# Kernel optimization log

Measured on AMD Instinct MI355X. Metric: run time of the kernel, lower is better.

Reference implementation:

```python
import jax, jax.numpy as jnp
import numpy as np

N, E, B, D, F_IN, E_IN, H = 8192, 32768, 256, 64, 11, 5, 128


def setup_inputs() -> dict:
    key = jax.random.key(0)
    ks = jax.random.split(key, 32)
    rn = lambda k, shape, s: jax.random.normal(k, shape, jnp.float32) * s
    inp = {
        'x': jax.random.normal(ks[0], (N, F_IN), jnp.float32),
        'edge_attr': jax.random.uniform(ks[1], (E, E_IN), jnp.float32),
        'lin0_w': rn(ks[2], (D, F_IN), 0.3), 'lin0_b': jnp.zeros((D,), jnp.float32),
        'nn1_w': rn(ks[3], (H, E_IN), 0.4), 'nn1_b': jnp.zeros((H,), jnp.float32),
        'nn2_w': rn(ks[4], (D * D, H), 0.05), 'nn2_b': jnp.zeros((D * D,), jnp.float32),
        'root_w': rn(ks[5], (D, D), 0.125), 'conv_b': jnp.zeros((D,), jnp.float32),
        'gru_w_ih': rn(ks[6], (3 * D, D), 0.125), 'gru_w_hh': rn(ks[7], (3 * D, D), 0.125),
        'gru_b_ih': jnp.zeros((3 * D,), jnp.float32), 'gru_b_hh': jnp.zeros((3 * D,), jnp.float32),
        's2s_w_ih': rn(ks[8], (4 * D, 2 * D), 0.1), 's2s_w_hh': rn(ks[9], (4 * D, D), 0.125),
        's2s_b_ih': jnp.zeros((4 * D,), jnp.float32), 's2s_b_hh': jnp.zeros((4 * D,), jnp.float32),
        'lin1_w': rn(ks[10], (D, 2 * D), 0.1), 'lin1_b': jnp.zeros((D,), jnp.float32),
        'lin2_w': rn(ks[11], (1, D), 0.125), 'lin2_b': jnp.zeros((1,), jnp.float32),
        'edge_index': jax.random.randint(ks[12], (2, E), 0, N),
        'batch': jnp.sort(jax.random.randint(ks[13], (N,), 0, B)),
    }
    return inp


def _forward(x, edge_attr, lin0_w, lin0_b, nn1_w, nn1_b, nn2_w, nn2_b, root_w, conv_b,
             gru_w_ih, gru_w_hh, gru_b_ih, gru_b_hh, s2s_w_ih, s2s_w_hh, s2s_b_ih, s2s_b_hh,
             lin1_w, lin1_b, lin2_w, lin2_b, edge_index, batch):
    src, dst = edge_index[0], edge_index[1]
    # edge-conditioned weights: MLP(edge_attr) -> [E, D, D]; edge_attr is fixed,
    # so compute once (identical math to calling conv.nn each iteration)
    W_e = (jax.nn.relu(edge_attr @ nn1_w.T + nn1_b) @ nn2_w.T + nn2_b).reshape(E, D, D)
    deg = jax.ops.segment_sum(jnp.ones((E,), jnp.float32), dst, num_segments=N)
    inv_deg = jnp.where(deg > 0, 1.0 / jnp.maximum(deg, 1.0), 0.0)[:, None]  # [N,1]

    out = jax.nn.relu(x @ lin0_w.T + lin0_b)  # [N, D]
    h = out
    for _ in range(3):
        # NNConv: gather src features, per-edge matmul, scatter-mean to dst, + root + bias
        msg = jnp.einsum('ed,edf->ef', out[src], W_e)  # [E, D]
        agg = jax.ops.segment_sum(msg, dst, num_segments=N) * inv_deg
        m = jax.nn.relu(agg + out @ root_w.T + conv_b)
        # single-step GRU (torch GRU equations)
        gx = m @ gru_w_ih.T + gru_b_ih
        gh = h @ gru_w_hh.T + gru_b_hh
        xr, xz, xn = jnp.split(gx, 3, axis=-1)
        hr, hz, hn = jnp.split(gh, 3, axis=-1)
        r = jax.nn.sigmoid(xr + hr)
        z = jax.nn.sigmoid(xz + hz)
        n = jnp.tanh(xn + r * hn)
        h = (1.0 - z) * n + z * h
        out = h

    # Set2Set pooling, 3 processing steps
    qh = jnp.zeros((B, D), jnp.float32)
    qc = jnp.zeros((B, D), jnp.float32)
    q_star = jnp.zeros((B, 2 * D), jnp.float32)
    for _ in range(3):
        gates = q_star @ s2s_w_ih.T + s2s_b_ih + qh @ s2s_w_hh.T + s2s_b_hh
        gi, gf, gg, go = jnp.split(gates, 4, axis=-1)
        qc = jax.nn.sigmoid(gf) * qc + jax.nn.sigmoid(gi) * jnp.tanh(gg)
        qh = jax.nn.sigmoid(go) * jnp.tanh(qc)
        q = qh  # [B, D]
        e = jnp.sum(out * q[batch], axis=-1)  # [N]
        emax = jax.ops.segment_max(e, batch, num_segments=B)
        emax = jnp.where(jnp.isfinite(emax), emax, 0.0)
        a = jnp.exp(e - emax[batch])
        a_sum = jax.ops.segment_sum(a, batch, num_segments=B)
        a = a / jnp.maximum(a_sum, 1e-12)[batch]
        r_vec = jax.ops.segment_sum(a[:, None] * out, batch, num_segments=B)  # [B, D]
        q_star = jnp.concatenate([q, r_vec], axis=-1)

    y = jax.nn.relu(q_star @ lin1_w.T + lin1_b) @ lin2_w.T + lin2_b
    return y.reshape(-1)  # [B]


def reference(x, edge_attr, lin0_w, lin0_b, nn1_w, nn1_b, nn2_w, nn2_b, root_w, conv_b,
              gru_w_ih, gru_w_hh, gru_b_ih, gru_b_hh, s2s_w_ih, s2s_w_hh, s2s_b_ih, s2s_b_hh,
              lin1_w, lin1_b, lin2_w, lin2_b, edge_index, batch):
    return _forward(x, edge_attr, lin0_w, lin0_b, nn1_w, nn1_b, nn2_w, nn2_b, root_w, conv_b,
                    gru_w_ih, gru_w_hh, gru_b_ih, gru_b_hh, s2s_w_ih, s2s_w_hh, s2s_b_ih, s2s_b_hh,
                    lin1_w, lin1_b, lin2_w, lin2_b, edge_index, batch)
```

## Files before the change

kernel.cpp:

```cpp
#include <hip/hip_runtime.h>
#include <hip/hip_bf16.h>
#include <stdint.h>

#define NN 8192
#define EE 32768
#define BB 256
#define DD 64
#define FIN 11
#define EIN 5
#define HH 128

typedef __attribute__((ext_vector_type(4))) float f32x4;
typedef __attribute__((ext_vector_type(8))) short bf16x8;

__device__ __forceinline__ float sigmoidf_(float x) { return 1.0f / (1.0f + expf(-x)); }

__device__ __forceinline__ void gload16(const void* g, void* l) {
    __builtin_amdgcn_global_load_lds(
        (const __attribute__((address_space(1))) unsigned int*)g,
        (__attribute__((address_space(3))) unsigned int*)l, 16, 0, 0);
}

__global__ __launch_bounds__(256) void k_setup(const float* __restrict__ x,
                                               const float* __restrict__ edge_attr,
                                               const float* __restrict__ lin0_w,
                                               const float* __restrict__ lin0_b,
                                               const float* __restrict__ nn1_w,
                                               const float* __restrict__ nn1_b,
                                               const float* __restrict__ nn2_w,
                                               const float* __restrict__ nn2b,
                                               const float* __restrict__ root_w,
                                               const float* __restrict__ whh,
                                               const float* __restrict__ bhh,
                                               const float* __restrict__ s2s_wih,
                                               const float* __restrict__ s2s_whh,
                                               const int* __restrict__ ei,
                                               const int* __restrict__ batch,
                                               __hip_bfloat16* __restrict__ h1,
                                               float* __restrict__ outN,
                                               __hip_bfloat16* __restrict__ nn2T,
                                               float* __restrict__ wihT,
                                               float* __restrict__ whhT,
                                               float* __restrict__ Bcat,
                                               float* __restrict__ bcat,
                                               int* __restrict__ deg,
                                               int* __restrict__ cnt) {
    const int bid = blockIdx.x, t = threadIdx.x;
    if (bid < 4096) {
        int u = bid * 256 + t;
        int e = u >> 5, k0 = (u & 31) * 4;
        float ea0 = edge_attr[e * EIN + 0], ea1 = edge_attr[e * EIN + 1],
              ea2 = edge_attr[e * EIN + 2], ea3 = edge_attr[e * EIN + 3],
              ea4 = edge_attr[e * EIN + 4];
        ushort4 o;
#pragma unroll
        for (int kk = 0; kk < 4; kk++) {
            int k = k0 + kk;
            const float* wr = nn1_w + k * EIN;
            float a = nn1_b[k] + ea0 * wr[0] + ea1 * wr[1] + ea2 * wr[2] + ea3 * wr[3] + ea4 * wr[4];
            __hip_bfloat16 b = __float2bfloat16(fmaxf(a, 0.0f));
            ((ushort*)&o)[kk] = *(ushort*)&b;
        }
        *(ushort4*)((ushort*)h1 + (size_t)e * 128 + k0) = o;
    } else if (bid < 4608) {
        int u = (bid - 4096) * 256 + t;
        int n = u >> 4, d0 = (u & 15) * 4;
        float xv[FIN];
#pragma unroll
        for (int k = 0; k < FIN; k++) xv[k] = x[n * FIN + k];
        float4 o;
#pragma unroll
        for (int dd = 0; dd < 4; dd++) {
            int d = d0 + dd;
            const float* wr = lin0_w + d * FIN;
            float a = lin0_b[d];
#pragma unroll
            for (int k = 0; k < FIN; k++) a += xv[k] * wr[k];
            ((float*)&o)[dd] = fmaxf(a, 0.0f);
        }
        *(float4*)(outN + (size_t)n * 64 + d0) = o;
    } else if (bid < 4864) {
        int u = (bid - 4608) * 256 + t;
        int d = u >> 10, rem = u & 1023, slot = rem >> 6, f = rem & 63;
        const float* src = nn2_w + ((size_t)(d * 64 + f) * 128 + slot * 8);
        float4 v0 = *(const float4*)(src);
        float4 v1 = *(const float4*)(src + 4);
        union { bf16x8 v; ushort us[8]; } ov;
        __hip_bfloat16 b;
        b = __float2bfloat16(v0.x); ov.us[0] = *(ushort*)&b;
        b = __float2bfloat16(v0.y); ov.us[1] = *(ushort*)&b;
        b = __float2bfloat16(v0.z); ov.us[2] = *(ushort*)&b;
        b = __float2bfloat16(v0.w); ov.us[3] = *(ushort*)&b;
        b = __float2bfloat16(v1.x); ov.us[4] = *(ushort*)&b;
        b = __float2bfloat16(v1.y); ov.us[5] = *(ushort*)&b;
        b = __float2bfloat16(v1.z); ov.us[6] = *(ushort*)&b;
        b = __float2bfloat16(v1.w); ov.us[7] = *(ushort*)&b;
        *(bf16x8*)((ushort*)nn2T + (size_t)u * 8) = ov.v;
    } else if (bid < 5056) {
        int i = (bid - 4864) * 256 + t;
        if (i < 256 * 128) {
            int j = i >> 7, k = i & 127;
            wihT[k * 256 + j] = s2s_wih[i];
        } else {
            int i2 = i - 256 * 128;
            if (i2 < 256 * 64) {
                int j = i2 >> 6, k = i2 & 63;
                whhT[k * 256 + j] = s2s_whh[i2];
            }
        }
    } else if (bid < 5136) {
        int i = (bid - 5056) * 256 + t;
        int r = i >> 6, c = i & 63;
        float v;
        if (r < 64) v = root_w[i];
        else if (r < 256) v = whh[(size_t)(r - 64) * 64 + c];
        else v = nn2b[c * 64 + (r - 256)];
        Bcat[i] = v;
        if (c == 0) bcat[r] = (r >= 64 && r < 256) ? bhh[r - 64] : 0.0f;
    } else {
        int i = (bid - 5136) * 256 + t;
        if (i < EE) atomicAdd(&deg[ei[EE + i]], 1);
        if (i < NN) atomicAdd(&cnt[batch[i]], 1);
    }
}

__global__ __launch_bounds__(256) void k_invscan(const int* __restrict__ deg,
                                                 float* __restrict__ invd,
                                                 const int* __restrict__ cnt,
                                                 int* __restrict__ offs) {
    const int bid = blockIdx.x, t = threadIdx.x;
    if (bid < 32) {
        int n = bid * 256 + t;
        int d = deg[n];
        invd[n] = d > 0 ? 1.0f / (float)d : 0.0f;
    } else {
        __shared__ int s[256];
        s[t] = cnt[t];
        __syncthreads();
        for (int off = 1; off < 256; off <<= 1) {
            int v = (t >= off) ? s[t - off] : 0;
            __syncthreads();
            s[t] += v;
            __syncthreads();
        }
        offs[t + 1] = s[t];
        if (t == 0) offs[0] = 0;
    }
}

__global__ __launch_bounds__(512, 4) void k_wemsg(const __hip_bfloat16* __restrict__ h1,
                                                  const __hip_bfloat16* __restrict__ nn2T,
                                                  const float* __restrict__ outN,
                                                  const float* __restrict__ rgh,
                                                  const int* __restrict__ ei,
                                                  const float* __restrict__ invd,
                                                  float* __restrict__ agg) {
    __shared__ ushort sB[2][64 * 128];
    __shared__ float soT[32][128];
    __shared__ int sDst[128];
    __shared__ int sSrc[128];
    __shared__ float sIv[128];

    const int t = threadIdx.x;
    const int w = t >> 6, l = t & 63;
    const int q = l >> 4, l15 = l & 15;
    const int eh = w >> 2, fs = (w & 3) * 16;
    const int e0 = (blockIdx.x >> 1) * 128;
    const int dh = blockIdx.x & 1;
    const int cbase = dh * 32;

    {
        int r = t >> 2, seg = t & 3;
        int s_ = ei[e0 + r];
        const float* orow = outN + (size_t)s_ * 64 + dh * 32 + seg * 8;
        float4 v0 = *(const float4*)(orow);
        float4 v1 = *(const float4*)(orow + 4);
        int c0 = seg * 8;
        soT[c0 + 0][r] = v0.x;
        soT[c0 + 1][r] = v0.y;
        soT[c0 + 2][r] = v0.z;
        soT[c0 + 3][r] = v0.w;
        soT[c0 + 4][r] = v1.x;
        soT[c0 + 5][r] = v1.y;
        soT[c0 + 6][r] = v1.z;
        soT[c0 + 7][r] = v1.w;
        if (seg == 0) {
            int d_ = ei[EE + e0 + r];
            sDst[r] = d_;
            sIv[r] = invd[d_];
            sSrc[r] = s_;
        }
    }
    bf16x8 af[4][4];
#pragma unroll
    for (int mi = 0; mi < 4; mi++)
#pragma unroll
        for (int kk = 0; kk < 4; kk++)
            af[mi][kk] = *(const bf16x8*)(h1 + (size_t)(e0 + eh * 64 + mi * 16 + l15) * 128 + (kk * 4 + q) * 8);

    const __hip_bfloat16* p0 = nn2T + (size_t)cbase * 8192 + (size_t)t * 8;
    const __hip_bfloat16* p1 = nn2T + (size_t)cbase * 8192 + (size_t)(512 + t) * 8;
    ushort* d0a = &sB[0][(w * 64) * 8];
    ushort* d0b = &sB[0][(512 + w * 64) * 8];
    ushort* d1a = &sB[1][(w * 64) * 8];
    ushort* d1b = &sB[1][(512 + w * 64) * 8];

    gload16(p0, d0a);
    gload16(p1, d0b);
    __syncthreads();

    float msg[4][4];
#pragma unroll
    for (int mi = 0; mi < 4; mi++)
#pragma unroll
        for (int j = 0; j < 4; j++) msg[mi][j] = 0.0f;

    const int rb = fs + l15;
    const int lo0 = ((0 * 4 + q) * 64 + rb) * 8;
    const int lo1 = ((1 * 4 + q) * 64 + rb) * 8;
    const int lo2 = ((2 * 4 + q) * 64 + rb) * 8;
    const int lo3 = ((3 * 4 + q) * 64 + rb) * 8;

    for (int dl = 0; dl < 32; ++dl) {
        const int cur = dl & 1;
        if (dl < 31) {
            size_t off = (size_t)(dl + 1) * 8192;
            gload16(p0 + off, cur ? d0a : d1a);
            gload16(p1 + off, cur ? d0b : d1b);
        }
        const ushort* sbc = &sB[cur][0];
        f32x4 a0 = (f32x4)0.0f, a1 = (f32x4)0.0f, a2 = (f32x4)0.0f, a3 = (f32x4)0.0f;
        {
            bf16x8 b0_ = *(const bf16x8*)&sbc[lo0];
            a0 = __builtin_amdgcn_mfma_f32_16x16x32_bf16(af[0][0], b0_, a0, 0, 0, 0);
            a1 = __builtin_amdgcn_mfma_f32_16x16x32_bf16(af[1][0], b0_, a1, 0, 0, 0);
            a2 = __builtin_amdgcn_mfma_f32_16x16x32_bf16(af[2][0], b0_, a2, 0, 0, 0);
            a3 = __builtin_amdgcn_mfma_f32_16x16x32_bf16(af[3][0], b0_, a3, 0, 0, 0);
            bf16x8 b1_ = *(const bf16x8*)&sbc[lo1];
            a0 = __builtin_amdgcn_mfma_f32_16x16x32_bf16(af[0][1], b1_, a0, 0, 0, 0);
            a1 = __builtin_amdgcn_mfma_f32_16x16x32_bf16(af[1][1], b1_, a1, 0, 0, 0);
            a2 = __builtin_amdgcn_mfma_f32_16x16x32_bf16(af[2][1], b1_, a2, 0, 0, 0);
            a3 = __builtin_amdgcn_mfma_f32_16x16x32_bf16(af[3][1], b1_, a3, 0, 0, 0);
            bf16x8 b2_ = *(const bf16x8*)&sbc[lo2];
            a0 = __builtin_amdgcn_mfma_f32_16x16x32_bf16(af[0][2], b2_, a0, 0, 0, 0);
            a1 = __builtin_amdgcn_mfma_f32_16x16x32_bf16(af[1][2], b2_, a1, 0, 0, 0);
            a2 = __builtin_amdgcn_mfma_f32_16x16x32_bf16(af[2][2], b2_, a2, 0, 0, 0);
            a3 = __builtin_amdgcn_mfma_f32_16x16x32_bf16(af[3][2], b2_, a3, 0, 0, 0);
            bf16x8 b3_ = *(const bf16x8*)&sbc[lo3];
            a0 = __builtin_amdgcn_mfma_f32_16x16x32_bf16(af[0][3], b3_, a0, 0, 0, 0);
            a1 = __builtin_amdgcn_mfma_f32_16x16x32_bf16(af[1][3], b3_, a1, 0, 0, 0);
            a2 = __builtin_amdgcn_mfma_f32_16x16x32_bf16(af[2][3], b3_, a2, 0, 0, 0);
            a3 = __builtin_amdgcn_mfma_f32_16x16x32_bf16(af[3][3], b3_, a3, 0, 0, 0);
        }
        {
            f32x4 s0 = *(const f32x4*)&soT[dl][eh * 64 + 0 * 16 + q * 4];
            f32x4 s1 = *(const f32x4*)&soT[dl][eh * 64 + 1 * 16 + q * 4];
            f32x4 s2 = *(const f32x4*)&soT[dl][eh * 64 + 2 * 16 + q * 4];
            f32x4 s3 = *(const f32x4*)&soT[dl][eh * 64 + 3 * 16 + q * 4];
#pragma unroll
            for (int j = 0; j < 4; j++) {
                msg[0][j] += a0[j] * s0[j];
                msg[1][j] += a1[j] * s1[j];
                msg[2][j] += a2[j] * s2[j];
                msg[3][j] += a3[j] * s3[j];
            }
        }
        __syncthreads();
    }

    const int fcol = fs + l15;
#pragma unroll
    for (int mi = 0; mi < 4; mi++) {
#pragma unroll
        for (int j = 0; j < 4; j++) {
            int er = eh * 64 + mi * 16 + q * 4 + j;
            float v = msg[mi][j];
            if (dh == 0) v += rgh[(size_t)sSrc[er] * 320 + 256 + fcol];
            atomicAdd(&agg[(size_t)sDst[er] * 64 + fcol], v * sIv[er]);
        }
    }
}

__global__ __launch_bounds__(256) void k_rgh(const float* __restrict__ A,
                                             const float* __restrict__ Bm,
                                             const float* __restrict__ bias,
                                             float* __restrict__ C,
                                             float* __restrict__ aggz) {
    const int tid = threadIdx.x;
    const int bx = blockIdx.x, by = blockIdx.y;
    {
        int bid = by * 5 + bx;
        if (bid < 512) {
            float4 z; z.x = z.y = z.z = z.w = 0.0f;
            *(float4*)(aggz + (size_t)bid * 1024 + tid * 4) = z;
        }
    }
    __shared__ float sA[64 * 68];
    __shared__ float sB[64 * 68];
    const float* Ab = A + (size_t)by * 64 * 64;
    const float* Bb = Bm + (size_t)bx * 64 * 64;
    for (int fi = tid; fi < 64 * 16; fi += 256) {
        int r = fi >> 4, c = (fi & 15) * 4;
        *(float4*)&sA[r * 68 + c] = *(const float4*)(Ab + (size_t)r * 64 + c);
        *(float4*)&sB[r * 68 + c] = *(const float4*)(Bb + (size_t)r * 64 + c);
    }
    __syncthreads();
    const int tx = tid & 15, ty = tid >> 4;
    float acc[4][4];
#pragma unroll
    for (int i = 0; i < 4; i++)
#pragma unroll
        for (int j = 0; j < 4; j++) acc[i][j] = 0.0f;
    for (int k = 0; k < 64; k += 4) {
        float4 av[4], bv[4];
#pragma unroll
        for (int i = 0; i < 4; i++) av[i] = *(const float4*)&sA[(ty + 16 * i) * 68 + k];
#pragma unroll
        for (int j = 0; j < 4; j++) bv[j] = *(const float4*)&sB[(tx + 16 * j) * 68 + k];
#pragma unroll
        for (int i = 0; i < 4; i++)
#pragma unroll
            for (int j = 0; j < 4; j++) {
                acc[i][j] += av[i].x * bv[j].x;
                acc[i][j] += av[i].y * bv[j].y;
                acc[i][j] += av[i].z * bv[j].z;
                acc[i][j] += av[i].w * bv[j].w;
            }
    }
#pragma unroll
    for (int i = 0; i < 4; i++) {
        size_t row = (size_t)by * 64 + ty + 16 * i;
#pragma unroll
        for (int j = 0; j < 4; j++) {
            int col = bx * 64 + tx + 16 * j;
            C[row * 320 + col] = acc[i][j] + bias[col];
        }
    }
}

__global__ __launch_bounds__(256) void k_gxgru(const float* __restrict__ agg,
                                               const float* __restrict__ rgh,
                                               const float* __restrict__ cb,
                                               const float* __restrict__ wih,
                                               const float* __restrict__ bih,
                                               float* __restrict__ outN) {
    __shared__ float sA[64 * 68];
    __shared__ float sB[192 * 68];
    const int t = threadIdx.x;
    const int by = blockIdx.x;
    for (int fi = t; fi < 64 * 16; fi += 256) {
        int r = fi >> 4, c = (fi & 15) * 4;
        float4 av = *(const float4*)(agg + (size_t)(by * 64 + r) * 64 + c);
        float4 rv = *(const float4*)(rgh + (size_t)(by * 64 + r) * 320 + c);
        float4 cv = *(const float4*)(cb + c);
        float4 m;
        m.x = fmaxf(av.x + rv.x + cv.x, 0.0f);
        m.y = fmaxf(av.y + rv.y + cv.y, 0.0f);
        m.z = fmaxf(av.z + rv.z + cv.z, 0.0f);
        m.w = fmaxf(av.w + rv.w + cv.w, 0.0f);
        *(float4*)&sA[r * 68 + c] = m;
    }
    for (int fi = t; fi < 192 * 16; fi += 256) {
        int r = fi >> 4, c = (fi & 15) * 4;
        *(float4*)&sB[r * 68 + c] = *(const float4*)(wih + (size_t)r * 64 + c);
    }
    __syncthreads();
    const int tx = t & 15, ty = t >> 4;
    float acc[3][4][4];
#pragma unroll
    for (int cx = 0; cx < 3; cx++)
#pragma unroll
        for (int i = 0; i < 4; i++)
#pragma unroll
            for (int j = 0; j < 4; j++) acc[cx][i][j] = 0.0f;
    for (int k = 0; k < 64; k += 4) {
        float4 av[4];
#pragma unroll
        for (int i = 0; i < 4; i++) av[i] = *(const float4*)&sA[(ty + 16 * i) * 68 + k];
#pragma unroll
        for (int cx = 0; cx < 3; cx++) {
            float4 bv[4];
#pragma unroll
            for (int j = 0; j < 4; j++) bv[j] = *(const float4*)&sB[(cx * 64 + tx + 16 * j) * 68 + k];
#pragma unroll
            for (int i = 0; i < 4; i++)
#pragma unroll
                for (int j = 0; j < 4; j++) {
                    acc[cx][i][j] += av[i].x * bv[j].x;
                    acc[cx][i][j] += av[i].y * bv[j].y;
                    acc[cx][i][j] += av[i].z * bv[j].z;
                    acc[cx][i][j] += av[i].w * bv[j].w;
                }
        }
    }
#pragma unroll
    for (int i = 0; i < 4; i++) {
        int n = by * 64 + ty + 16 * i;
        const float* ghr = rgh + (size_t)n * 320 + 64;
#pragma unroll
        for (int j = 0; j < 4; j++) {
            int d = tx + 16 * j;
            float r = sigmoidf_(acc[0][i][j] + bih[d] + ghr[d]);
            float z = sigmoidf_(acc[1][i][j] + bih[64 + d] + ghr[64 + d]);
            float nn_ = tanhf(acc[2][i][j] + bih[128 + d] + r * ghr[128 + d]);
            float hp = outN[(size_t)n * 64 + d];
            outN[(size_t)n * 64 + d] = (1.0f - z) * nn_ + z * hp;
        }
    }
}

__global__ __launch_bounds__(256) void k_s2sall(const float* __restrict__ outN,
                                                const int* __restrict__ offs,
                                                const float* __restrict__ wihT,
                                                const float* __restrict__ whhT,
                                                const float* __restrict__ bih,
                                                const float* __restrict__ bhh,
                                                const float* __restrict__ lin1_w,
                                                const float* __restrict__ lin1_b,
                                                const float* __restrict__ lin2_w,
                                                const float* __restrict__ lin2_b,
                                                float* __restrict__ earr,
                                                float* __restrict__ y) {
    const int b = blockIdx.x, t = threadIdx.x;
    const int w = t >> 6, l = t & 63;
    __shared__ float qs[128], qhL[64], qcL[64], gates[256];
    __shared__ float red[8];
    __shared__ float rpart[4][64];
    __shared__ float hbuf[64];
    const int s0 = offs[b], s1 = offs[b + 1];
    if (t < 128) qs[t] = 0.0f;
    if (t < 64) { qhL[t] = 0.0f; qcL[t] = 0.0f; }
    __syncthreads();

    for (int st = 0; st < 3; st++) {
        float g = bih[t] + bhh[t];
        for (int k = 0; k < 128; k++) g += qs[k] * wihT[k * 256 + t];
        for (int k = 0; k < 64; k++) g += qhL[k] * whhT[k * 256 + t];
        gates[t] = g;
        __syncthreads();
        if (t < 64) {
            float gi = gates[t], gf = gates[64 + t], gg = gates[128 + t], go = gates[192 + t];
            float c = sigmoidf_(gf) * qcL[t] + sigmoidf_(gi) * tanhf(gg);
            qcL[t] = c;
            qhL[t] = sigmoidf_(go) * tanhf(c);
        }
        __syncthreads();
        float mx = -INFINITY;
        for (int i = s0 + w; i < s1; i += 4) {
            float p = outN[(size_t)i * 64 + l] * qhL[l];
#pragma unroll
            for (int o = 32; o > 0; o >>= 1) p += __shfl_xor(p, o, 64);
            if (l == 0) earr[i] = p;
            mx = fmaxf(mx, p);
        }
        if (l == 0) red[w] = mx;
        __syncthreads();
        mx = fmaxf(fmaxf(red[0], red[1]), fmaxf(red[2], red[3]));
        if (!isfinite(mx)) mx = 0.0f;
        float sm = 0.0f, racc = 0.0f;
        for (int i = s0 + w; i < s1; i += 4) {
            float a = expf(earr[i] - mx);
            sm += a;
            racc += a * outN[(size_t)i * 64 + l];
        }
        rpart[w][l] = racc;
        if (l == 0) red[4 + w] = sm;
        __syncthreads();
        float smT = fmaxf(red[4] + red[5] + red[6] + red[7], 1e-12f);
        if (t < 64) {
            float r = (rpart[0][t] + rpart[1][t] + rpart[2][t] + rpart[3][t]) / smT;
            qs[t] = qhL[t];
            qs[64 + t] = r;
        }
        __syncthreads();
    }
    if (t < 64) {
        float h = lin1_b[t];
        for (int k = 0; k < 128; k++) h += qs[k] * lin1_w[t * 128 + k];
        hbuf[t] = fmaxf(h, 0.0f) * lin2_w[t];
    }
    __syncthreads();
    if (w == 0) {
        float p = hbuf[l];
#pragma unroll
        for (int o = 32; o > 0; o >>= 1) p += __shfl_xor(p, o, 64);
        if (l == 0) y[b] = p + lin2_b[0];
    }
}

extern "C" void kernel_launch(void* const* d_in, const int* in_sizes, int n_in,
                              void* d_out, int out_size, void* d_ws, size_t ws_size,
                              hipStream_t stream) {
    const float* x = (const float*)d_in[0];
    const float* edge_attr = (const float*)d_in[1];
    const float* lin0_w = (const float*)d_in[2];
    const float* lin0_b = (const float*)d_in[3];
    const float* nn1_w = (const float*)d_in[4];
    const float* nn1_b = (const float*)d_in[5];
    const float* nn2_w = (const float*)d_in[6];
    const float* nn2_b = (const float*)d_in[7];
    const float* root_w = (const float*)d_in[8];
    const float* conv_b = (const float*)d_in[9];
    const float* gru_w_ih = (const float*)d_in[10];
    const float* gru_w_hh = (const float*)d_in[11];
    const float* gru_b_ih = (const float*)d_in[12];
    const float* gru_b_hh = (const float*)d_in[13];
    const float* s2s_w_ih = (const float*)d_in[14];
    const float* s2s_w_hh = (const float*)d_in[15];
    const float* s2s_b_ih = (const float*)d_in[16];
    const float* s2s_b_hh = (const float*)d_in[17];
    const float* lin1_w = (const float*)d_in[18];
    const float* lin1_b = (const float*)d_in[19];
    const float* lin2_w = (const float*)d_in[20];
    const float* lin2_b = (const float*)d_in[21];
    const int* ei = (const int*)d_in[22];
    const int* batch = (const int*)d_in[23];
    float* outp = (float*)d_out;

    char* w = (char*)d_ws;
    auto carve = [&](size_t bytes) { char* p = w; w += (bytes + 255) & ~(size_t)255; return p; };
    __hip_bfloat16* nn2T = (__hip_bfloat16*)carve((size_t)4096 * 128 * 2);
    float* outN = (float*)carve((size_t)NN * 64 * 4);
    __hip_bfloat16* h1 = (__hip_bfloat16*)carve((size_t)EE * 128 * 2);
    int* deg = (int*)carve(NN * 4);
    float* invd = (float*)carve(NN * 4);
    float* agg = (float*)carve((size_t)NN * 64 * 4);
    float* rgh = (float*)carve((size_t)NN * 320 * 4);
    float* Bcat = (float*)carve((size_t)320 * 64 * 4);
    float* bcat = (float*)carve(320 * 4);
    float* wihT = (float*)carve((size_t)128 * 256 * 4);
    float* whhT = (float*)carve((size_t)64 * 256 * 4);
    float* earr = (float*)carve(NN * 4);
    int* cnt = (int*)carve(256 * 4);
    int* offs = (int*)carve(257 * 4);

    hipMemsetAsync(deg, 0, NN * 4, stream);
    hipMemsetAsync(cnt, 0, 256 * 4, stream);

    k_setup<<<5264, 256, 0, stream>>>(x, edge_attr, lin0_w, lin0_b, nn1_w, nn1_b,
                                      nn2_w, nn2_b, root_w, gru_w_hh, gru_b_hh,
                                      s2s_w_ih, s2s_w_hh, ei, batch,
                                      h1, outN, nn2T, wihT, whhT, Bcat, bcat, deg, cnt);
    k_invscan<<<33, 256, 0, stream>>>(deg, invd, cnt, offs);

    for (int it = 0; it < 3; it++) {
        k_rgh<<<dim3(5, NN / 64), 256, 0, stream>>>(outN, Bcat, bcat, rgh, agg);
        k_wemsg<<<EE / 64, 512, 0, stream>>>(h1, nn2T, outN, rgh, ei, invd, agg);
        k_gxgru<<<NN / 64, 256, 0, stream>>>(agg, rgh, conv_b, gru_w_ih, gru_b_ih, outN);
    }

    k_s2sall<<<BB, 256, 0, stream>>>(outN, offs, wihT, whhT, s2s_b_ih, s2s_b_hh,
                                     lin1_w, lin1_b, lin2_w, lin2_b, earr, outp);
}
```

Baseline: 293.6 us.

## Fuse next-iteration rgh GEMM into GRU kernel and split wemsg over four column groups

The per-iteration k_rgh launch is removed. After the GRU update, k_gxgru keeps the new hidden tile in LDS, computes the next iteration's rgh projection itself, and zeroes agg as it reads it. One k_rgh launch is kept before the loop. k_wemsg now splits output columns into four 16-wide groups instead of two 32-wide ones, which halves its LDS staging and raises the occupancy hint to 6. Its B-fragment loads are hoisted ahead of the MFMAs, which now run under s_setprio. This saves launches and a round trip of outN through global memory, at the cost of more work and extra syncs inside k_gxgru, and four-fold reuse of each edge tile's A-fragment loads.

```diff
diff --git a/kernel.cpp b/kernel.cpp
--- a/kernel.cpp
+++ b/kernel.cpp
@@ -148,7 +148,7 @@
     }
 }
 
-__global__ __launch_bounds__(512, 4) void k_wemsg(const __hip_bfloat16* __restrict__ h1,
+__global__ __launch_bounds__(512, 6) void k_wemsg(const __hip_bfloat16* __restrict__ h1,
                                                   const __hip_bfloat16* __restrict__ nn2T,
                                                   const float* __restrict__ outN,
                                                   const float* __restrict__ rgh,
@@ -156,7 +156,7 @@
                                                   const float* __restrict__ invd,
                                                   float* __restrict__ agg) {
     __shared__ ushort sB[2][64 * 128];
-    __shared__ float soT[32][128];
+    __shared__ float soT[16][128];
     __shared__ int sDst[128];
     __shared__ int sSrc[128];
     __shared__ float sIv[128];
@@ -165,25 +165,19 @@
     const int w = t >> 6, l = t & 63;
     const int q = l >> 4, l15 = l & 15;
     const int eh = w >> 2, fs = (w & 3) * 16;
-    const int e0 = (blockIdx.x >> 1) * 128;
-    const int dh = blockIdx.x & 1;
-    const int cbase = dh * 32;
+    const int e0 = (blockIdx.x >> 2) * 128;
+    const int dh = blockIdx.x & 3;
+    const int cbase = dh * 16;
 
     {
         int r = t >> 2, seg = t & 3;
         int s_ = ei[e0 + r];
-        const float* orow = outN + (size_t)s_ * 64 + dh * 32 + seg * 8;
-        float4 v0 = *(const float4*)(orow);
-        float4 v1 = *(const float4*)(orow + 4);
-        int c0 = seg * 8;
-        soT[c0 + 0][r] = v0.x;
-        soT[c0 + 1][r] = v0.y;
-        soT[c0 + 2][r] = v0.z;
-        soT[c0 + 3][r] = v0.w;
-        soT[c0 + 4][r] = v1.x;
-        soT[c0 + 5][r] = v1.y;
-        soT[c0 + 6][r] = v1.z;
-        soT[c0 + 7][r] = v1.w;
+        float4 v = *(const float4*)(outN + (size_t)s_ * 64 + dh * 16 + seg * 4);
+        int c0 = seg * 4;
+        soT[c0 + 0][r] = v.x;
+        soT[c0 + 1][r] = v.y;
+        soT[c0 + 2][r] = v.z;
+        soT[c0 + 3][r] = v.w;
         if (seg == 0) {
             int d_ = ei[EE + e0 + r];
             sDst[r] = d_;
@@ -221,37 +215,39 @@
     const int lo2 = ((2 * 4 + q) * 64 + rb) * 8;
     const int lo3 = ((3 * 4 + q) * 64 + rb) * 8;
 
-    for (int dl = 0; dl < 32; ++dl) {
+    for (int dl = 0; dl < 16; ++dl) {
         const int cur = dl & 1;
-        if (dl < 31) {
+        if (dl < 15) {
             size_t off = (size_t)(dl + 1) * 8192;
             gload16(p0 + off, cur ? d0a : d1a);
             gload16(p1 + off, cur ? d0b : d1b);
         }
         const ushort* sbc = &sB[cur][0];
         f32x4 a0 = (f32x4)0.0f, a1 = (f32x4)0.0f, a2 = (f32x4)0.0f, a3 = (f32x4)0.0f;
+        bf16x8 b0_ = *(const bf16x8*)&sbc[lo0];
+        bf16x8 b1_ = *(const bf16x8*)&sbc[lo1];
+        bf16x8 b2_ = *(const bf16x8*)&sbc[lo2];
+        bf16x8 b3_ = *(const bf16x8*)&sbc[lo3];
+        __builtin_amdgcn_s_setprio(1);
         {
-            bf16x8 b0_ = *(const bf16x8*)&sbc[lo0];
             a0 = __builtin_amdgcn_mfma_f32_16x16x32_bf16(af[0][0], b0_, a0, 0, 0, 0);
             a1 = __builtin_amdgcn_mfma_f32_16x16x32_bf16(af[1][0], b0_, a1, 0, 0, 0);
             a2 = __builtin_amdgcn_mfma_f32_16x16x32_bf16(af[2][0], b0_, a2, 0, 0, 0);
             a3 = __builtin_amdgcn_mfma_f32_16x16x32_bf16(af[3][0], b0_, a3, 0, 0, 0);
-            bf16x8 b1_ = *(const bf16x8*)&sbc[lo1];
             a0 = __builtin_amdgcn_mfma_f32_16x16x32_bf16(af[0][1], b1_, a0, 0, 0, 0);
             a1 = __builtin_amdgcn_mfma_f32_16x16x32_bf16(af[1][1], b1_, a1, 0, 0, 0);
             a2 = __builtin_amdgcn_mfma_f32_16x16x32_bf16(af[2][1], b1_, a2, 0, 0, 0);
             a3 = __builtin_amdgcn_mfma_f32_16x16x32_bf16(af[3][1], b1_, a3, 0, 0, 0);
-            bf16x8 b2_ = *(const bf16x8*)&sbc[lo2];
             a0 = __builtin_amdgcn_mfma_f32_16x16x32_bf16(af[0][2], b2_, a0, 0, 0, 0);
             a1 = __builtin_amdgcn_mfma_f32_16x16x32_bf16(af[1][2], b2_, a1, 0, 0, 0);
             a2 = __builtin_amdgcn_mfma_f32_16x16x32_bf16(af[2][2], b2_, a2, 0, 0, 0);
             a3 = __builtin_amdgcn_mfma_f32_16x16x32_bf16(af[3][2], b2_, a3, 0, 0, 0);
-            bf16x8 b3_ = *(const bf16x8*)&sbc[lo3];
             a0 = __builtin_amdgcn_mfma_f32_16x16x32_bf16(af[0][3], b3_, a0, 0, 0, 0);
             a1 = __builtin_amdgcn_mfma_f32_16x16x32_bf16(af[1][3], b3_, a1, 0, 0, 0);
             a2 = __builtin_amdgcn_mfma_f32_16x16x32_bf16(af[2][3], b3_, a2, 0, 0, 0);
             a3 = __builtin_amdgcn_mfma_f32_16x16x32_bf16(af[3][3], b3_, a3, 0, 0, 0);
         }
+        __builtin_amdgcn_s_setprio(0);
         {
             f32x4 s0 = *(const f32x4*)&soT[dl][eh * 64 + 0 * 16 + q * 4];
             f32x4 s1 = *(const f32x4*)&soT[dl][eh * 64 + 1 * 16 + q * 4];
@@ -338,11 +334,14 @@
     }
 }
 
-__global__ __launch_bounds__(256) void k_gxgru(const float* __restrict__ agg,
-                                               const float* __restrict__ rgh,
+__global__ __launch_bounds__(256) void k_gxgru(float* __restrict__ agg,
+                                               float* __restrict__ rgh,
                                                const float* __restrict__ cb,
                                                const float* __restrict__ wih,
                                                const float* __restrict__ bih,
+                                               const float* __restrict__ Bcat,
+                                               const float* __restrict__ bcat,
+                                               const int do_rgh,
                                                float* __restrict__ outN) {
     __shared__ float sA[64 * 68];
     __shared__ float sB[192 * 68];
@@ -350,7 +349,8 @@
     const int by = blockIdx.x;
     for (int fi = t; fi < 64 * 16; fi += 256) {
         int r = fi >> 4, c = (fi & 15) * 4;
-        float4 av = *(const float4*)(agg + (size_t)(by * 64 + r) * 64 + c);
+        float* ap = agg + (size_t)(by * 64 + r) * 64 + c;
+        float4 av = *(const float4*)ap;
         float4 rv = *(const float4*)(rgh + (size_t)(by * 64 + r) * 320 + c);
         float4 cv = *(const float4*)(cb + c);
         float4 m;
@@ -359,6 +359,8 @@
         m.z = fmaxf(av.z + rv.z + cv.z, 0.0f);
         m.w = fmaxf(av.w + rv.w + cv.w, 0.0f);
         *(float4*)&sA[r * 68 + c] = m;
+        float4 z; z.x = z.y = z.z = z.w = 0.0f;
+        *(float4*)ap = z;
     }
     for (int fi = t; fi < 192 * 16; fi += 256) {
         int r = fi >> 4, c = (fi & 15) * 4;
@@ -393,6 +395,7 @@
                 }
         }
     }
+    __syncthreads();
 #pragma unroll
     for (int i = 0; i < 4; i++) {
         int n = by * 64 + ty + 16 * i;
@@ -404,7 +407,50 @@
             float z = sigmoidf_(acc[1][i][j] + bih[64 + d] + ghr[64 + d]);
             float nn_ = tanhf(acc[2][i][j] + bih[128 + d] + r * ghr[128 + d]);
             float hp = outN[(size_t)n * 64 + d];
-            outN[(size_t)n * 64 + d] = (1.0f - z) * nn_ + z * hp;
+            float hnew = (1.0f - z) * nn_ + z * hp;
+            outN[(size_t)n * 64 + d] = hnew;
+            sA[(ty + 16 * i) * 68 + d] = hnew;
+        }
+    }
+    if (do_rgh) {
+        __syncthreads();
+        for (int cx = 0; cx < 5; cx++) {
+            for (int fi = t; fi < 64 * 16; fi += 256) {
+                int r = fi >> 4, c = (fi & 15) * 4;
+                *(float4*)&sB[r * 68 + c] = *(const float4*)(Bcat + (size_t)(cx * 64 + r) * 64 + c);
+            }
+            __syncthreads();
+            float a2[4][4];
+#pragma unroll
+            for (int i = 0; i < 4; i++)
+#pragma unroll
+                for (int j = 0; j < 4; j++) a2[i][j] = 0.0f;
+            for (int k = 0; k < 64; k += 4) {
+                float4 av[4], bv[4];
+#pragma unroll
+                for (int i = 0; i < 4; i++) av[i] = *(const float4*)&sA[(ty + 16 * i) * 68 + k];
+#pragma unroll
+                for (int j = 0; j < 4; j++) bv[j] = *(const float4*)&sB[(tx + 16 * j) * 68 + k];
+#pragma unroll
+                for (int i = 0; i < 4; i++)
+#pragma unroll
+                    for (int j = 0; j < 4; j++) {
+                        a2[i][j] += av[i].x * bv[j].x;
+                        a2[i][j] += av[i].y * bv[j].y;
+                        a2[i][j] += av[i].z * bv[j].z;
+                        a2[i][j] += av[i].w * bv[j].w;
+                    }
+            }
+#pragma unroll
+            for (int i = 0; i < 4; i++) {
+                size_t row = (size_t)by * 64 + ty + 16 * i;
+#pragma unroll
+                for (int j = 0; j < 4; j++) {
+                    int col = cx * 64 + tx + 16 * j;
+                    rgh[row * 320 + col] = a2[i][j] + bcat[col];
+                }
+            }
+            __syncthreads();
         }
     }
 }
@@ -542,11 +588,12 @@
                                       s2s_w_ih, s2s_w_hh, ei, batch,
                                       h1, outN, nn2T, wihT, whhT, Bcat, bcat, deg, cnt);
     k_invscan<<<33, 256, 0, stream>>>(deg, invd, cnt, offs);
+    k_rgh<<<dim3(5, NN / 64), 256, 0, stream>>>(outN, Bcat, bcat, rgh, agg);
 
     for (int it = 0; it < 3; it++) {
-        k_rgh<<<dim3(5, NN / 64), 256, 0, stream>>>(outN, Bcat, bcat, rgh, agg);
-        k_wemsg<<<EE / 64, 512, 0, stream>>>(h1, nn2T, outN, rgh, ei, invd, agg);
-        k_gxgru<<<NN / 64, 256, 0, stream>>>(agg, rgh, conv_b, gru_w_ih, gru_b_ih, outN);
+        k_wemsg<<<(EE / 128) * 4, 512, 0, stream>>>(h1, nn2T, outN, rgh, ei, invd, agg);
+        k_gxgru<<<NN / 64, 256, 0, stream>>>(agg, rgh, conv_b, gru_w_ih, gru_b_ih,
+                                             Bcat, bcat, (it < 2) ? 1 : 0, outN);
     }
 
     k_s2sall<<<BB, 256, 0, stream>>>(outN, offs, wihT, whhT, s2s_b_ih, s2s_b_hh,
```

New measurement: 928.6 us. 216% more time.
